# Optimization experiments

Hardware: AMD Instinct MI355X
Metric: run time of the kernel (lower is better)

The kernel has to match this reference:

```python
import jax, jax.numpy as jnp
import numpy as np

N = 2048


def setup_inputs() -> dict:
    key = jax.random.key(0)
    k1, k2 = jax.random.split(key)
    input1 = jax.random.normal(k1, (N, N), dtype=jnp.float32)
    input2 = jax.random.normal(k2, (N, N), dtype=jnp.float32)
    return {"input1": input1, "input2": input2}


def reference(input1, input2):
    # Common subexpressions (the original recomputes these many times;
    # the math is identical):
    A = input1 @ input1            # mm(input1, input1)
    B = input1 @ input2            # mm(input1, input2)
    C = input2 @ B                 # mm(input2, mm(input1, input2))
    D = input2 @ A                 # mm(input2, mm(input1, input1))

    t1 = A
    t2 = A @ input2 + B
    t3 = C + B @ A
    t4 = C @ A + D @ input2
    t5 = (C @ A) @ A + (D @ B) @ A
    t6 = t1 - (t2 + t3 * t4 / t5)
    return t6
```

## Files before the change

kernel.cpp:

```cpp
#include <hip/hip_runtime.h>


#define NMAT 2048

constexpr int FM = 128, FN = 128, FK = 16;
constexpr int LDA = FM + 4;
constexpr int LDB = FN + 4;
constexpr int KCHUNK = 512;

__global__ __launch_bounds__(256) void sgemm_chunk(
    const float* __restrict__ Am, const float* __restrict__ Bm,
    float* __restrict__ Pm) {
  __shared__ float As[FK][LDA];
  __shared__ float Bs[FK][LDB];
  const int tid = threadIdx.x;
  const int row0 = blockIdx.y * FM;
  const int col0 = blockIdx.x * FN;
  const int kb = blockIdx.z * KCHUNK;
  const int ty = tid >> 4;
  const int tx = tid & 15;

  const int ar = tid >> 2;
  const int ac = (tid & 3) * 4;
  const int bk = tid >> 5;
  const int bc = (tid & 31) * 4;

  float acc[8][8] = {};
  float4 va0, va1, vb0, vb1;

  const float* pa0 = &Am[(size_t)(row0 + ar) * NMAT + kb + ac];
  const float* pa1 = pa0 + (size_t)64 * NMAT;
  const float* pb0 = &Bm[(size_t)(kb + bk) * NMAT + col0 + bc];
  const float* pb1 = pb0 + (size_t)8 * NMAT;

  va0 = *(const float4*)pa0;
  va1 = *(const float4*)pa1;
  vb0 = *(const float4*)pb0;
  vb1 = *(const float4*)pb1;

#pragma unroll 1
  for (int t = 0; t < KCHUNK / FK; ++t) {
    __syncthreads();
    As[ac + 0][ar] = va0.x;
    As[ac + 1][ar] = va0.y;
    As[ac + 2][ar] = va0.z;
    As[ac + 3][ar] = va0.w;
    As[ac + 0][ar + 64] = va1.x;
    As[ac + 1][ar + 64] = va1.y;
    As[ac + 2][ar + 64] = va1.z;
    As[ac + 3][ar + 64] = va1.w;
    *(float4*)&Bs[bk][bc] = vb0;
    *(float4*)&Bs[bk + 8][bc] = vb1;
    __syncthreads();

    if (t + 1 < KCHUNK / FK) {
      pa0 += FK;
      pa1 += FK;
      pb0 += (size_t)FK * NMAT;
      pb1 += (size_t)FK * NMAT;
      va0 = *(const float4*)pa0;
      va1 = *(const float4*)pa1;
      vb0 = *(const float4*)pb0;
      vb1 = *(const float4*)pb1;
    }

#pragma unroll
    for (int k = 0; k < FK; ++k) {
      const float4 a0 = *(const float4*)&As[k][ty * 4];
      const float4 a1 = *(const float4*)&As[k][64 + ty * 4];
      const float4 b0 = *(const float4*)&Bs[k][tx * 4];
      const float4 b1 = *(const float4*)&Bs[k][64 + tx * 4];
      const float af[8] = {a0.x, a0.y, a0.z, a0.w, a1.x, a1.y, a1.z, a1.w};
      const float bf[8] = {b0.x, b0.y, b0.z, b0.w, b1.x, b1.y, b1.z, b1.w};
#pragma unroll
      for (int i = 0; i < 8; ++i)
#pragma unroll
        for (int j = 0; j < 8; ++j)
          acc[i][j] = fmaf(af[i], bf[j], acc[i][j]);
    }
  }

  float* dst = Pm + (size_t)blockIdx.z * NMAT * NMAT;
#pragma unroll
  for (int i = 0; i < 8; ++i) {
    const int r = row0 + ((i < 4) ? (ty * 4 + i) : (64 + ty * 4 + (i - 4)));
#pragma unroll
    for (int jb = 0; jb < 2; ++jb) {
      const int c = col0 + ((jb == 0) ? (tx * 4) : (64 + tx * 4));
      float4 v;
      v.x = acc[i][jb * 4 + 0];
      v.y = acc[i][jb * 4 + 1];
      v.z = acc[i][jb * 4 + 2];
      v.w = acc[i][jb * 4 + 3];
      *(float4*)&dst[(size_t)r * NMAT + c] = v;
    }
  }
}

template <int DO_ADD>
__global__ __launch_bounds__(256) void reduce_k4(
    const float* __restrict__ Pm, const float* __restrict__ Addm,
    float* __restrict__ outp) {
  const size_t NN = (size_t)NMAT * NMAT;
  const size_t i = ((size_t)blockIdx.x * 256 + threadIdx.x) * 4;
  const float4 c0 = *(const float4*)&Pm[i];
  const float4 c1 = *(const float4*)&Pm[i + NN];
  const float4 c2 = *(const float4*)&Pm[i + 2 * NN];
  const float4 c3 = *(const float4*)&Pm[i + 3 * NN];
  float4 v;
  v.x = __fadd_rn(__fadd_rn(__fadd_rn(__fadd_rn(0.0f, c0.x), c1.x), c2.x), c3.x);
  v.y = __fadd_rn(__fadd_rn(__fadd_rn(__fadd_rn(0.0f, c0.y), c1.y), c2.y), c3.y);
  v.z = __fadd_rn(__fadd_rn(__fadd_rn(__fadd_rn(0.0f, c0.z), c1.z), c2.z), c3.z);
  v.w = __fadd_rn(__fadd_rn(__fadd_rn(__fadd_rn(0.0f, c0.w), c1.w), c2.w), c3.w);
  if (DO_ADD) {
    const float4 ad = *(const float4*)&Addm[i];
    v.x = __fadd_rn(v.x, ad.x);
    v.y = __fadd_rn(v.y, ad.y);
    v.z = __fadd_rn(v.z, ad.z);
    v.w = __fadd_rn(v.w, ad.w);
  }
  *(float4*)&outp[i] = v;
}

template <int DO_ADD>
__global__ __launch_bounds__(256) void sgemm512(
    const float* __restrict__ Am, const float* __restrict__ Bm, float* Cm,
    const float* Addm) {
  __shared__ float As[FK][LDA];
  __shared__ float Bs[FK][LDB];
  const int tid = threadIdx.x;
  const int row0 = blockIdx.y * FM;
  const int col0 = blockIdx.x * FN;
  const int ty = tid >> 4;
  const int tx = tid & 15;
  const int ar = tid >> 2;
  const int ac = (tid & 3) * 4;
  const int bk = tid >> 5;
  const int bc = (tid & 31) * 4;

  float tot[8][8] = {};
  float acc[8][8] = {};
  float4 va0, va1, vb0, vb1;

  va0 = *(const float4*)&Am[(size_t)(row0 + ar) * NMAT + ac];
  va1 = *(const float4*)&Am[(size_t)(row0 + ar + 64) * NMAT + ac];
  vb0 = *(const float4*)&Bm[(size_t)bk * NMAT + col0 + bc];
  vb1 = *(const float4*)&Bm[(size_t)(bk + 8) * NMAT + col0 + bc];

  for (int k0 = 0; k0 < NMAT; k0 += FK) {
    __syncthreads();
    As[ac + 0][ar] = va0.x;
    As[ac + 1][ar] = va0.y;
    As[ac + 2][ar] = va0.z;
    As[ac + 3][ar] = va0.w;
    As[ac + 0][ar + 64] = va1.x;
    As[ac + 1][ar + 64] = va1.y;
    As[ac + 2][ar + 64] = va1.z;
    As[ac + 3][ar + 64] = va1.w;
    *(float4*)&Bs[bk][bc] = vb0;
    *(float4*)&Bs[bk + 8][bc] = vb1;
    __syncthreads();

    if (k0 + FK < NMAT) {
      const int kn = k0 + FK;
      va0 = *(const float4*)&Am[(size_t)(row0 + ar) * NMAT + kn + ac];
      va1 = *(const float4*)&Am[(size_t)(row0 + ar + 64) * NMAT + kn + ac];
      vb0 = *(const float4*)&Bm[(size_t)(kn + bk) * NMAT + col0 + bc];
      vb1 = *(const float4*)&Bm[(size_t)(kn + bk + 8) * NMAT + col0 + bc];
    }

#pragma unroll
    for (int k = 0; k < FK; ++k) {
      const float4 a0 = *(const float4*)&As[k][ty * 4];
      const float4 a1 = *(const float4*)&As[k][64 + ty * 4];
      const float4 b0 = *(const float4*)&Bs[k][tx * 4];
      const float4 b1 = *(const float4*)&Bs[k][64 + tx * 4];
      const float af[8] = {a0.x, a0.y, a0.z, a0.w, a1.x, a1.y, a1.z, a1.w};
      const float bf[8] = {b0.x, b0.y, b0.z, b0.w, b1.x, b1.y, b1.z, b1.w};
#pragma unroll
      for (int i = 0; i < 8; ++i)
#pragma unroll
        for (int j = 0; j < 8; ++j)
          acc[i][j] = fmaf(af[i], bf[j], acc[i][j]);
    }

    if (((k0 + FK) & 511) == 0) {
#pragma unroll
      for (int i = 0; i < 8; ++i)
#pragma unroll
        for (int j = 0; j < 8; ++j) {
          tot[i][j] = __fadd_rn(tot[i][j], acc[i][j]);
          acc[i][j] = 0.0f;
        }
    }
  }

#pragma unroll
  for (int i = 0; i < 8; ++i) {
    const int r = row0 + ((i < 4) ? (ty * 4 + i) : (64 + ty * 4 + (i - 4)));
#pragma unroll
    for (int jb = 0; jb < 2; ++jb) {
      const int c = col0 + ((jb == 0) ? (tx * 4) : (64 + tx * 4));
      const size_t idx = (size_t)r * NMAT + c;
      float4 v;
      v.x = tot[i][jb * 4 + 0];
      v.y = tot[i][jb * 4 + 1];
      v.z = tot[i][jb * 4 + 2];
      v.w = tot[i][jb * 4 + 3];
      if (DO_ADD) {
        const float4 ad = *(const float4*)&Addm[idx];
        v.x = __fadd_rn(v.x, ad.x);
        v.y = __fadd_rn(v.y, ad.y);
        v.z = __fadd_rn(v.z, ad.z);
        v.w = __fadd_rn(v.w, ad.w);
      }
      *(float4*)&Cm[idx] = v;
    }
  }
}

__global__ __launch_bounds__(256) void final_fp32(
    const float* __restrict__ t1, const float* __restrict__ t2,
    const float* t3, const float* __restrict__ t4,
    const float* __restrict__ t5, float* outp) {
  size_t i = (size_t)blockIdx.x * 256 + threadIdx.x;
  float num = __fmul_rn(t3[i], t4[i]);
  float q = __fdiv_rn(num, t5[i]);
  float s = __fadd_rn(t2[i], q);
  outp[i] = __fsub_rn(t1[i], s);
}

extern "C" void kernel_launch(void* const* d_in, const int* in_sizes, int n_in,
                              void* d_out, int out_size, void* d_ws,
                              size_t ws_size, hipStream_t stream) {
  const float* X1 = (const float*)d_in[0];
  const float* X2 = (const float*)d_in[1];
  float* out = (float*)d_out;

  const size_t NN = (size_t)NMAT * NMAT;
  const size_t M32 = NN * sizeof(float);
  char* w = (char*)d_ws;
  float* fA  = (float*)(w + 0 * M32);
  float* fB  = (float*)(w + 1 * M32);
  float* fC  = (float*)(w + 2 * M32);
  float* fD  = (float*)(w + 3 * M32);
  float* fP  = (float*)(w + 4 * M32);
  float* fQ  = (float*)(w + 5 * M32);
  float* t2f = (float*)(w + 6 * M32);
  float* t4f = (float*)(w + 7 * M32);
  float* fT  = (float*)(w + 2 * M32);
  float* t5f = (float*)(w + 3 * M32);

  dim3 blk(256);
  dim3 ew((unsigned)(NN / 256));

  if (ws_size >= 12 * M32) {
    float* Pk = (float*)(w + 8 * M32);
    dim3 gsk(NMAT / FN, NMAT / FM, 4);
    dim3 gr((unsigned)(NN / (256 * 4)));

    auto gemm = [&](const float* A, const float* B, float* dst,
                    const float* add) {
      sgemm_chunk<<<gsk, blk, 0, stream>>>(A, B, Pk);
      if (add)
        reduce_k4<1><<<gr, blk, 0, stream>>>(Pk, add, dst);
      else
        reduce_k4<0><<<gr, blk, 0, stream>>>(Pk, nullptr, dst);
    };

    gemm(X1, X1, fA, nullptr);
    gemm(X1, X2, fB, nullptr);
    gemm(X2, fB, fC, nullptr);
    gemm(X2, fA, fD, nullptr);
    gemm(fC, fA, fP, nullptr);
    gemm(fD, fB, fQ, nullptr);
    gemm(fB, fA, out, fC);
    gemm(fD, X2, t4f, fP);
    gemm(fA, X2, t2f, fB);
    gemm(fP, fA, fT, nullptr);
    gemm(fQ, fA, t5f, fT);
    final_fp32<<<ew, blk, 0, stream>>>(fA, t2f, out, t4f, t5f, out);
  } else {
    dim3 grid(NMAT / FN, NMAT / FM);
    sgemm512<0><<<grid, blk, 0, stream>>>(X1, X1, fA, nullptr);
    sgemm512<0><<<grid, blk, 0, stream>>>(X1, X2, fB, nullptr);
    sgemm512<0><<<grid, blk, 0, stream>>>(X2, fB, fC, nullptr);
    sgemm512<0><<<grid, blk, 0, stream>>>(X2, fA, fD, nullptr);
    sgemm512<0><<<grid, blk, 0, stream>>>(fC, fA, fP, nullptr);
    sgemm512<0><<<grid, blk, 0, stream>>>(fD, fB, fQ, nullptr);
    sgemm512<1><<<grid, blk, 0, stream>>>(fB, fA, out, fC);
    sgemm512<1><<<grid, blk, 0, stream>>>(fD, X2, t4f, fP);
    sgemm512<1><<<grid, blk, 0, stream>>>(fA, X2, t2f, fB);
    sgemm512<0><<<grid, blk, 0, stream>>>(fP, fA, fT, nullptr);
    sgemm512<1><<<grid, blk, 0, stream>>>(fQ, fA, t5f, fT);
    final_fp32<<<ew, blk, 0, stream>>>(fA, t2f, out, t4f, t5f, out);
  }
}
```

Measured before the change: 2.350 ms.

## Enlarge split-K GEMM tile to 256x128 with double-buffered LDS

Grows the split-K SGEMM block tile from 128x128 to 256x128, giving each thread a 16x8 accumulator. It adds double-buffered shared-memory staging with a two-step register prefetch, so each loop iteration needs one barrier instead of two. The goal is more FMAs per shared-memory load and less synchronisation stall. The cost is much higher register pressure (128 accumulators plus prefetch registers under launch_bounds(256,2)), twice the LDS per block, and half as many blocks (256 instead of 512), which lowers occupancy and may cause spills.

Result: slower. 2.420 ms (+3.0%).

```diff
diff --git a/kernel.cpp b/kernel.cpp
--- a/kernel.cpp
+++ b/kernel.cpp
@@ -3,19 +3,20 @@
 
 #define NMAT 2048
 
-constexpr int FM = 128, FN = 128, FK = 16;
-constexpr int LDA = FM + 4;
-constexpr int LDB = FN + 4;
+constexpr int FK = 16;
 constexpr int KCHUNK = 512;
-
-__global__ __launch_bounds__(256) void sgemm_chunk(
+constexpr int CM = 256, CN = 128;
+constexpr int LDA2 = CM + 4;
+constexpr int LDB2 = CN + 4;
+
+__global__ __launch_bounds__(256, 2) void sgemm_chunk(
     const float* __restrict__ Am, const float* __restrict__ Bm,
     float* __restrict__ Pm) {
-  __shared__ float As[FK][LDA];
-  __shared__ float Bs[FK][LDB];
+  __shared__ float As[2][FK][LDA2];
+  __shared__ float Bs[2][FK][LDB2];
   const int tid = threadIdx.x;
-  const int row0 = blockIdx.y * FM;
-  const int col0 = blockIdx.x * FN;
+  const int row0 = blockIdx.y * CM;
+  const int col0 = blockIdx.x * CN;
   const int kb = blockIdx.z * KCHUNK;
   const int ty = tid >> 4;
   const int tx = tid & 15;
@@ -25,68 +26,95 @@
   const int bk = tid >> 5;
   const int bc = (tid & 31) * 4;
 
-  float acc[8][8] = {};
-  float4 va0, va1, vb0, vb1;
-
-  const float* pa0 = &Am[(size_t)(row0 + ar) * NMAT + kb + ac];
-  const float* pa1 = pa0 + (size_t)64 * NMAT;
-  const float* pb0 = &Bm[(size_t)(kb + bk) * NMAT + col0 + bc];
-  const float* pb1 = pb0 + (size_t)8 * NMAT;
-
-  va0 = *(const float4*)pa0;
-  va1 = *(const float4*)pa1;
-  vb0 = *(const float4*)pb0;
-  vb1 = *(const float4*)pb1;
+  float acc[16][8] = {};
+  float4 va[4], vb[2];
+
+  const float* pa = &Am[(size_t)(row0 + ar) * NMAT + kb + ac];
+  const float* pb = &Bm[(size_t)(kb + bk) * NMAT + col0 + bc];
+
+  constexpr int NT = KCHUNK / FK;
+
+#pragma unroll
+  for (int p = 0; p < 4; ++p)
+    va[p] = *(const float4*)(pa + (size_t)(64 * p) * NMAT);
+#pragma unroll
+  for (int p = 0; p < 2; ++p)
+    vb[p] = *(const float4*)(pb + (size_t)(8 * p) * NMAT);
+#pragma unroll
+  for (int p = 0; p < 4; ++p) {
+    As[0][ac + 0][ar + 64 * p] = va[p].x;
+    As[0][ac + 1][ar + 64 * p] = va[p].y;
+    As[0][ac + 2][ar + 64 * p] = va[p].z;
+    As[0][ac + 3][ar + 64 * p] = va[p].w;
+  }
+#pragma unroll
+  for (int p = 0; p < 2; ++p)
+    *(float4*)&Bs[0][bk + 8 * p][bc] = vb[p];
+  pa += FK;
+  pb += (size_t)FK * NMAT;
+#pragma unroll
+  for (int p = 0; p < 4; ++p)
+    va[p] = *(const float4*)(pa + (size_t)(64 * p) * NMAT);
+#pragma unroll
+  for (int p = 0; p < 2; ++p)
+    vb[p] = *(const float4*)(pb + (size_t)(8 * p) * NMAT);
+  __syncthreads();
 
 #pragma unroll 1
-  for (int t = 0; t < KCHUNK / FK; ++t) {
-    __syncthreads();
-    As[ac + 0][ar] = va0.x;
-    As[ac + 1][ar] = va0.y;
-    As[ac + 2][ar] = va0.z;
-    As[ac + 3][ar] = va0.w;
-    As[ac + 0][ar + 64] = va1.x;
-    As[ac + 1][ar + 64] = va1.y;
-    As[ac + 2][ar + 64] = va1.z;
-    As[ac + 3][ar + 64] = va1.w;
-    *(float4*)&Bs[bk][bc] = vb0;
-    *(float4*)&Bs[bk + 8][bc] = vb1;
-    __syncthreads();
-
-    if (t + 1 < KCHUNK / FK) {
-      pa0 += FK;
-      pa1 += FK;
-      pb0 += (size_t)FK * NMAT;
-      pb1 += (size_t)FK * NMAT;
-      va0 = *(const float4*)pa0;
-      va1 = *(const float4*)pa1;
-      vb0 = *(const float4*)pb0;
-      vb1 = *(const float4*)pb1;
+  for (int t = 0; t < NT; ++t) {
+    const int cur = t & 1;
+    const int nxt = cur ^ 1;
+
+    if (t + 1 < NT) {
+#pragma unroll
+      for (int p = 0; p < 4; ++p) {
+        As[nxt][ac + 0][ar + 64 * p] = va[p].x;
+        As[nxt][ac + 1][ar + 64 * p] = va[p].y;
+        As[nxt][ac + 2][ar + 64 * p] = va[p].z;
+        As[nxt][ac + 3][ar + 64 * p] = va[p].w;
+      }
+#pragma unroll
+      for (int p = 0; p < 2; ++p)
+        *(float4*)&Bs[nxt][bk + 8 * p][bc] = vb[p];
+    }
+    if (t + 2 < NT) {
+      pa += FK;
+      pb += (size_t)FK * NMAT;
+#pragma unroll
+      for (int p = 0; p < 4; ++p)
+        va[p] = *(const float4*)(pa + (size_t)(64 * p) * NMAT);
+#pragma unroll
+      for (int p = 0; p < 2; ++p)
+        vb[p] = *(const float4*)(pb + (size_t)(8 * p) * NMAT);
     }
 
 #pragma unroll
     for (int k = 0; k < FK; ++k) {
-      const float4 a0 = *(const float4*)&As[k][ty * 4];
-      const float4 a1 = *(const float4*)&As[k][64 + ty * 4];
-      const float4 b0 = *(const float4*)&Bs[k][tx * 4];
-      const float4 b1 = *(const float4*)&Bs[k][64 + tx * 4];
-      const float af[8] = {a0.x, a0.y, a0.z, a0.w, a1.x, a1.y, a1.z, a1.w};
+      float4 a0 = *(const float4*)&As[cur][k][ty * 4];
+      float4 a1 = *(const float4*)&As[cur][k][64 + ty * 4];
+      float4 a2 = *(const float4*)&As[cur][k][128 + ty * 4];
+      float4 a3 = *(const float4*)&As[cur][k][192 + ty * 4];
+      float4 b0 = *(const float4*)&Bs[cur][k][tx * 4];
+      float4 b1 = *(const float4*)&Bs[cur][k][64 + tx * 4];
+      const float af[16] = {a0.x, a0.y, a0.z, a0.w, a1.x, a1.y, a1.z, a1.w,
+                            a2.x, a2.y, a2.z, a2.w, a3.x, a3.y, a3.z, a3.w};
       const float bf[8] = {b0.x, b0.y, b0.z, b0.w, b1.x, b1.y, b1.z, b1.w};
 #pragma unroll
-      for (int i = 0; i < 8; ++i)
+      for (int i = 0; i < 16; ++i)
 #pragma unroll
         for (int j = 0; j < 8; ++j)
           acc[i][j] = fmaf(af[i], bf[j], acc[i][j]);
     }
+    __syncthreads();
   }
 
   float* dst = Pm + (size_t)blockIdx.z * NMAT * NMAT;
 #pragma unroll
-  for (int i = 0; i < 8; ++i) {
-    const int r = row0 + ((i < 4) ? (ty * 4 + i) : (64 + ty * 4 + (i - 4)));
+  for (int i = 0; i < 16; ++i) {
+    const int r = row0 + (i >> 2) * 64 + ty * 4 + (i & 3);
 #pragma unroll
     for (int jb = 0; jb < 2; ++jb) {
-      const int c = col0 + ((jb == 0) ? (tx * 4) : (64 + tx * 4));
+      const int c = col0 + jb * 64 + tx * 4;
       float4 v;
       v.x = acc[i][jb * 4 + 0];
       v.y = acc[i][jb * 4 + 1];
@@ -122,6 +150,10 @@
   *(float4*)&outp[i] = v;
 }
 
+constexpr int FM = 128, FN = 128;
+constexpr int LDA = FM + 4;
+constexpr int LDB = FN + 4;
+
 template <int DO_ADD>
 __global__ __launch_bounds__(256) void sgemm512(
     const float* __restrict__ Am, const float* __restrict__ Bm, float* Cm,
@@ -256,7 +288,7 @@
 
   if (ws_size >= 12 * M32) {
     float* Pk = (float*)(w + 8 * M32);
-    dim3 gsk(NMAT / FN, NMAT / FM, 4);
+    dim3 gsk(NMAT / CN, NMAT / CM, 4);
     dim3 gr((unsigned)(NN / (256 * 4)));
 
     auto gemm = [&](const float* A, const float* B, float* dst,
```
